# Kernel tuning notes

Measured on AMD Instinct MI355X. Metric: run time of the kernel, lower is better.

## Reference

```python
import jax, jax.numpy as jnp
import numpy as np

E = 8        # n_routed_experts
K = 2        # n_experts_per_token
H = 1024     # d_hidden
D = 512      # d_expert
NSH = 2      # n_shared_experts -> shared expert width = D*NSH


def setup_inputs() -> dict:
    key = jax.random.key(0)
    ks = jax.random.split(key, 8)
    s = 0.02
    x = jax.random.normal(ks[0], (4, 2048, H), jnp.float32)
    W_router = (jax.random.normal(ks[1], (H, E), jnp.float32) * s)
    Wg = (jax.random.normal(ks[2], (E, H, D), jnp.float32) * s)   # per-expert gate proj
    Wu = (jax.random.normal(ks[3], (E, H, D), jnp.float32) * s)   # per-expert up proj
    Wd = (jax.random.normal(ks[4], (E, D, H), jnp.float32) * s)   # per-expert down proj
    Ds = D * NSH
    Wsg = (jax.random.normal(ks[5], (H, Ds), jnp.float32) * s)
    Wsu = (jax.random.normal(ks[6], (H, Ds), jnp.float32) * s)
    Wsd = (jax.random.normal(ks[7], (Ds, H), jnp.float32) * s)
    return {"x": x, "W_router": W_router, "Wg": Wg, "Wu": Wu, "Wd": Wd,
            "Wsg": Wsg, "Wsu": Wsu, "Wsd": Wsd}


def reference(x, W_router, Wg, Wu, Wd, Wsg, Wsu, Wsd):
    B, S, Hd = x.shape
    T = B * S
    xf = x.reshape(T, Hd)

    # shared expert (SwiGLU)
    shared = (jax.nn.silu(xf @ Wsg) * (xf @ Wsu)) @ Wsd          # [T, H]

    # gating: softmax -> top-k -> renormalize
    logits = xf @ W_router                                        # [T, E]
    probs = jax.nn.softmax(logits, axis=-1)
    topk_scores, topk_idx = jax.lax.top_k(probs, K)               # [T, K]
    topk_scores = topk_scores / jnp.sum(topk_scores, axis=-1, keepdims=True)

    # combine weights: zero for unselected experts (topk indices are distinct,
    # so the original's first-match score selection equals a simple scatter)
    combine = jnp.zeros((T, E), x.dtype).at[jnp.arange(T)[:, None], topk_idx].set(topk_scores)

    # per-expert SwiGLU, computed densely and combined with sparse weights
    gate = jax.nn.silu(jnp.einsum('th,ehd->etd', xf, Wg))         # [E, T, D]
    up = jnp.einsum('th,ehd->etd', xf, Wu)                        # [E, T, D]
    expert_out = jnp.einsum('etd,edh->eth', gate * up, Wd)        # [E, T, H]
    routed = jnp.einsum('eth,te->th', expert_out, combine)        # [T, H]

    out = (routed + shared).reshape(B, S, Hd)

    # load-balancing aux loss: E * sum(mean_probs^2)
    probs_mean = jnp.mean(probs.reshape(B, S, E), axis=(0, 1))
    aux_loss = E * jnp.sum(probs_mean * probs_mean)
    return out, aux_loss
```

## Files before the change

### kernel.cpp

```cpp
#include <hip/hip_runtime.h>


typedef unsigned short u16;
typedef unsigned int   u32;
typedef short short8 __attribute__((ext_vector_type(8)));
typedef float f32x4  __attribute__((ext_vector_type(4)));

#define AS1 __attribute__((address_space(1)))
#define AS3 __attribute__((address_space(3)))

constexpr int T  = 8192;
constexpr int H  = 1024;
constexpr int E  = 8;
constexpr int D  = 512;
constexpr int DS = 1024;
constexpr int PAIR_CAP  = 17408;
constexpr int MT_ROUTED = 136;
constexpr int RB = 256;

__device__ __forceinline__ u16 f2bf(float f){
  u32 u = __builtin_bit_cast(u32, f);
  u += 0x7fffu + ((u >> 16) & 1u);
  return (u16)(u >> 16);
}
__device__ __forceinline__ float bf2f(u16 h){
  u32 u = ((u32)h) << 16;
  return __builtin_bit_cast(float, u);
}

__device__ __forceinline__ void gl_lds16(const u16* g, u16* l){
  __builtin_amdgcn_global_load_lds((const AS1 void*)g, (AS3 void*)l, 16, 0, 0);
}

__device__ __forceinline__ void wait_vmcnt8(){ __builtin_amdgcn_s_waitcnt(0x0f78); }
__device__ __forceinline__ void wait_vmcnt0(){ __builtin_amdgcn_s_waitcnt(0x0f70); }

__device__ __forceinline__ void bar_sync(){
  __builtin_amdgcn_fence(__ATOMIC_RELEASE, "workgroup", "local");
  __builtin_amdgcn_s_barrier();
  __builtin_amdgcn_fence(__ATOMIC_ACQUIRE, "workgroup", "local");
}

__device__ __forceinline__ void xcd_remap(int& mtile, int& ntile){
  int NT = gridDim.x;
  int lid = blockIdx.y * NT + blockIdx.x;
  int x8 = lid & 7, s = lid >> 3;
  mtile = x8 + 8 * (s / NT);
  ntile = s % NT;
}

template<int ISS>
struct StagePtr { const u16* p[ISS]; };

template<int ROWS>
__device__ __forceinline__ void stage_init(StagePtr<ROWS/32>& sp,
    const u16* __restrict__ gbase, int ld, int rowbase,
    const int* __restrict__ gather, int wave, int lane){
  constexpr int ISS = ROWS / 32;
  int lr = lane >> 3, ch = lane & 7;
  int chs = (ch ^ lr) * 8;
#pragma unroll
  for (int j = 0; j < ISS; ++j){
    int idx = wave * ISS + j;
    int row = idx * 8 + lr;
    int grow = gather ? gather[rowbase + row] : (rowbase + row);
    sp.p[j] = gbase + (long)grow * ld + chs;
  }
}

template<int ROWS>
__device__ __forceinline__ void stage_issue(const StagePtr<ROWS/32>& sp, int k0,
                                            u16* lds, int wave, int lane){
  constexpr int ISS = ROWS / 32;
#pragma unroll
  for (int j = 0; j < ISS; ++j)
    gl_lds16(sp.p[j] + k0, lds + (wave * ISS + j) * 512);
}

__device__ __forceinline__ int swz_off(int c, int lane){
  return ((c ^ (lane & 7)) * 8);
}

__global__ void __launch_bounds__(256) router_kernel(
    const float* __restrict__ x, const float* __restrict__ Wr,
    u16* __restrict__ xb,
    int* __restrict__ topk_idx, float* __restrict__ topk_w,
    int* __restrict__ partial_hist, float* __restrict__ partial_probs)
{
  __shared__ int   hist_s[4][8];
  __shared__ float ps_s[4][8];
  int tid = threadIdx.x, lane = tid & 63, wv = tid >> 6;
  int   histl[8] = {0,0,0,0,0,0,0,0};
  float psl[8]   = {0.f,0.f,0.f,0.f,0.f,0.f,0.f,0.f};

  for (int it = 0; it < 8; ++it){
    int t = blockIdx.x * 32 + wv * 8 + it;
    const float4* xr = (const float4*)(x + (long)t * H);
    uint2* xbr = (uint2*)(xb + (long)t * H);
    float acc[8];
#pragma unroll
    for (int e = 0; e < 8; ++e) acc[e] = 0.f;
#pragma unroll
    for (int i = 0; i < 4; ++i){
      float4 xv = xr[i * 64 + lane];
      u32 lo = (u32)f2bf(xv.x) | ((u32)f2bf(xv.y) << 16);
      u32 hi = (u32)f2bf(xv.z) | ((u32)f2bf(xv.w) << 16);
      xbr[i * 64 + lane] = make_uint2(lo, hi);
      int h0 = i * 256 + lane * 4;
#pragma unroll
      for (int j = 0; j < 4; ++j){
        float xs = (j == 0) ? xv.x : (j == 1) ? xv.y : (j == 2) ? xv.z : xv.w;
        const float4* wr = (const float4*)(Wr + (long)(h0 + j) * E);
        float4 w0 = wr[0], w1 = wr[1];
        acc[0] += xs * w0.x; acc[1] += xs * w0.y; acc[2] += xs * w0.z; acc[3] += xs * w0.w;
        acc[4] += xs * w1.x; acc[5] += xs * w1.y; acc[6] += xs * w1.z; acc[7] += xs * w1.w;
      }
    }
#pragma unroll
    for (int off = 32; off >= 1; off >>= 1){
#pragma unroll
      for (int e = 0; e < 8; ++e) acc[e] += __shfl_xor(acc[e], off, 64);
    }
    if (lane == 0){
      float m = acc[0];
#pragma unroll
      for (int e = 1; e < 8; ++e) m = fmaxf(m, acc[e]);
      float p[8], s = 0.f;
#pragma unroll
      for (int e = 0; e < 8; ++e){ p[e] = __expf(acc[e] - m); s += p[e]; }
      float inv = 1.f / s;
#pragma unroll
      for (int e = 0; e < 8; ++e) psl[e] += p[e] * inv;
      int i1 = 0; float v1 = p[0];
#pragma unroll
      for (int e = 1; e < 8; ++e) if (p[e] > v1){ v1 = p[e]; i1 = e; }
      int i2 = -1; float v2 = -1.f;
#pragma unroll
      for (int e = 0; e < 8; ++e) if (e != i1 && p[e] > v2){ v2 = p[e]; i2 = e; }
      float rs = 1.f / (v1 + v2);
      topk_idx[2 * t] = i1; topk_idx[2 * t + 1] = i2;
      topk_w[2 * t] = v1 * rs; topk_w[2 * t + 1] = v2 * rs;
      histl[i1]++; histl[i2]++;
    }
  }
  if (lane == 0){
#pragma unroll
    for (int e = 0; e < 8; ++e){ hist_s[wv][e] = histl[e]; ps_s[wv][e] = psl[e]; }
  }
  __syncthreads();
  if (tid < 8){
    int hs = 0; float ps = 0.f;
#pragma unroll
    for (int w = 0; w < 4; ++w){ hs += hist_s[w][tid]; ps += ps_s[w][tid]; }
    partial_hist[blockIdx.x * 8 + tid]  = hs;
    partial_probs[blockIdx.x * 8 + tid] = ps;
  }
}

__global__ void __launch_bounds__(64) scan_kernel(
    const int* __restrict__ partial_hist, const float* __restrict__ partial_probs,
    int* __restrict__ block_offset, float* __restrict__ out_aux)
{
  __shared__ int   csum[8][8];
  __shared__ float cps[8][8];
  __shared__ int   cbase[8][8];
  __shared__ int   base_s[8];
  int tid = threadIdx.x, e = tid & 7, c = tid >> 3;
  int s = 0; float f = 0.f;
  for (int b = c * 32; b < c * 32 + 32; ++b){
    s += partial_hist[b * 8 + e]; f += partial_probs[b * 8 + e];
  }
  csum[c][e] = s; cps[c][e] = f;
  __syncthreads();
  if (tid < 8){
    int tot = 0;
    for (int cc = 0; cc < 8; ++cc){ cbase[cc][tid] = tot; tot += csum[cc][tid]; }
    csum[0][tid] = tot;
  }
  __syncthreads();
  if (tid == 0){
    int off = 0;
    for (int ee = 0; ee < 8; ++ee){ base_s[ee] = off; off += (csum[0][ee] + 127) & ~127; }
    float a = 0.f;
    for (int ee = 0; ee < 8; ++ee){
      float ps = 0.f;
      for (int cc = 0; cc < 8; ++cc) ps += cps[cc][ee];
      float m = ps * (1.f / (float)T);
      a += m * m;
    }
    out_aux[0] = (float)E * a;
  }
  __syncthreads();
  int run = base_s[e] + cbase[c][e];
  for (int b = c * 32; b < c * 32 + 32; ++b){
    block_offset[b * 8 + e] = run;
    run += partial_hist[b * 8 + e];
  }
}

__global__ void __launch_bounds__(64) scatter_kernel(
    const int* __restrict__ topk_idx, const float* __restrict__ topk_w,
    const int* __restrict__ block_offset,
    int* __restrict__ pair_token, int* __restrict__ pair_expert,
    float* __restrict__ pair_score, int* __restrict__ token_pos)
{
  int lane = threadIdx.x, b = blockIdx.x;
  int idx = b * 64 + lane;
  int t = idx >> 1;
  int e = topk_idx[idx];
  float w = topk_w[idx];
  unsigned long long below = lane ? ((1ull << lane) - 1ull) : 0ull;
  int rank = 0, basee = 0;
#pragma unroll
  for (int ee = 0; ee < 8; ++ee){
    unsigned long long m = __ballot(e == ee);
    if (e == ee){ rank = __popcll(m & below); basee = block_offset[b * 8 + ee]; }
  }
  int pos = basee + rank;
  pair_token[pos] = t;
  pair_expert[pos] = e;
  pair_score[pos] = w;
  token_pos[idx] = pos;
}

__device__ __forceinline__ void transpose_body(const float* src, u16* dst, int R, int C,
                                               int bz){
  __shared__ float tile[32][33];
  long zoff = (long)bz * R * C;
  int tx = threadIdx.x & 31, ty = threadIdx.x >> 5;
  int c = blockIdx.x * 32 + tx;
  int rb = blockIdx.y * 32;
#pragma unroll
  for (int j = 0; j < 4; ++j)
    tile[ty + j * 8][tx] = src[zoff + (long)(rb + ty + j * 8) * C + c];
  __syncthreads();
#pragma unroll
  for (int j = 0; j < 4; ++j){
    int cc = blockIdx.x * 32 + ty + j * 8;
    dst[zoff + (long)cc * R + rb + tx] = f2bf(tile[tx][ty + j * 8]);
  }
}

__global__ void __launch_bounds__(256) transpose_kernel(const float* __restrict__ src,
                                                        u16* __restrict__ dst, int R, int C){
  transpose_body(src, dst, R, C, blockIdx.z);
}

__global__ void __launch_bounds__(256) transpose2_kernel(
    const float* __restrict__ s0, u16* __restrict__ d0,
    const float* __restrict__ s1, u16* __restrict__ d1, int R, int C, int Z){
  int z = blockIdx.z;
  if (z < Z) transpose_body(s0, d0, R, C, z);
  else       transpose_body(s1, d1, R, C, z - Z);
}

__global__ void __launch_bounds__(256) transpose3_kernel(
    const float* __restrict__ s0, u16* __restrict__ d0,
    const float* __restrict__ s1, u16* __restrict__ d1,
    const float* __restrict__ s2, u16* __restrict__ d2, int R, int C){
  int z = blockIdx.z;
  const float* s = (z == 0) ? s0 : (z == 1) ? s1 : s2;
  u16* d = (z == 0) ? d0 : (z == 1) ? d1 : d2;
  transpose_body(s, d, R, C, 0);
}

__global__ void __launch_bounds__(256) gateup_kernel(
    const u16* __restrict__ A, const u16* __restrict__ Bg, const u16* __restrict__ Bu,
    u16* __restrict__ Hout, int N, int K,
    const int* __restrict__ gather, const int* __restrict__ pexp, long bstride)
{
  __shared__ u16 As[2][128 * 64];
  __shared__ u16 Bgs[2][64 * 64];
  __shared__ u16 Bus[2][64 * 64];
  int tid = threadIdx.x, lane = tid & 63, wave = tid >> 6;
  int wy = wave >> 1, wx = wave & 1;
  int mtile, ntile; xcd_remap(mtile, ntile);
  int m0 = mtile * 128, n0 = ntile * 64;
  int e = pexp ? pexp[m0] : 0;
  const u16* bg = Bg + (long)e * bstride;
  const u16* bu = Bu + (long)e * bstride;
  int rl = lane & 15, q = lane >> 4;

  StagePtr<4> spA; StagePtr<2> spG; StagePtr<2> spU;
  stage_init<128>(spA, A, K, m0, gather, wave, lane);
  stage_init<64>(spG, bg, K, n0, nullptr, wave, lane);
  stage_init<64>(spU, bu, K, n0, nullptr, wave, lane);

  f32x4 accG[4][2], accU[4][2];
#pragma unroll
  for (int i = 0; i < 4; ++i)
#pragma unroll
    for (int j = 0; j < 2; ++j)
#pragma unroll
      for (int r = 0; r < 4; ++r){ accG[i][j][r] = 0.f; accU[i][j][r] = 0.f; }

  stage_issue<128>(spA, 0, As[0], wave, lane);
  stage_issue<64>(spG, 0, Bgs[0], wave, lane);
  stage_issue<64>(spU, 0, Bus[0], wave, lane);

  int NI = K / 64;
  for (int i = 0; i < NI; ++i){
    int cur = i & 1, nxt = cur ^ 1;
    if (i + 1 < NI){
      int kn = (i + 1) * 64;
      stage_issue<128>(spA, kn, As[nxt], wave, lane);
      stage_issue<64>(spG, kn, Bgs[nxt], wave, lane);
      stage_issue<64>(spU, kn, Bus[nxt], wave, lane);
      wait_vmcnt8();
    } else {
      wait_vmcnt0();
    }
    bar_sync();
#pragma unroll
    for (int ks = 0; ks < 2; ++ks){
      int off = swz_off(ks * 4 + q, lane);
      short8 a[4], g2[2], u2[2];
#pragma unroll
      for (int mt = 0; mt < 4; ++mt)
        a[mt] = *(const short8*)(As[cur] + (wy * 64 + mt * 16 + rl) * 64 + off);
#pragma unroll
      for (int nt = 0; nt < 2; ++nt){
        g2[nt] = *(const short8*)(Bgs[cur] + (wx * 32 + nt * 16 + rl) * 64 + off);
        u2[nt] = *(const short8*)(Bus[cur] + (wx * 32 + nt * 16 + rl) * 64 + off);
      }
#pragma unroll
      for (int mt = 0; mt < 4; ++mt)
#pragma unroll
        for (int nt = 0; nt < 2; ++nt){
          accG[mt][nt] = __builtin_amdgcn_mfma_f32_16x16x32_bf16(a[mt], g2[nt], accG[mt][nt], 0, 0, 0);
          accU[mt][nt] = __builtin_amdgcn_mfma_f32_16x16x32_bf16(a[mt], u2[nt], accU[mt][nt], 0, 0, 0);
        }
    }
    if (i + 1 < NI) bar_sync();
  }
  int row0 = m0 + wy * 64, col0 = n0 + wx * 32;
#pragma unroll
  for (int mt = 0; mt < 4; ++mt)
#pragma unroll
    for (int nt = 0; nt < 2; ++nt)
#pragma unroll
      for (int r = 0; r < 4; ++r){
        int row = row0 + mt * 16 + q * 4 + r;
        int col = col0 + nt * 16 + rl;
        float g = accG[mt][nt][r], u = accU[mt][nt][r];
        float h = g / (1.f + __expf(-g)) * u;
        Hout[(long)row * N + col] = f2bf(h);
      }
}

template<bool ROUTED>
__device__ __forceinline__ void down_body(
    const u16* __restrict__ A, const u16* __restrict__ Bbase, int K,
    u16* __restrict__ rout, const float* __restrict__ pair_score,
    const int* __restrict__ token_pos, float* __restrict__ out)
{
  __shared__ u16 As[2][128 * 64];
  __shared__ u16 Bs[2][128 * 64];
  int tid = threadIdx.x, lane = tid & 63, wave = tid >> 6;
  int wy = wave >> 1, wx = wave & 1;
  int mtile, ntile; xcd_remap(mtile, ntile);
  int m0 = mtile * 128, n0 = ntile * 128;
  int rl = lane & 15, q = lane >> 4;

  StagePtr<4> spA, spB;
  stage_init<128>(spA, A, K, m0, nullptr, wave, lane);
  stage_init<128>(spB, Bbase, K, n0, nullptr, wave, lane);

  f32x4 acc[4][4];
#pragma unroll
  for (int i = 0; i < 4; ++i)
#pragma unroll
    for (int j = 0; j < 4; ++j)
#pragma unroll
      for (int r = 0; r < 4; ++r) acc[i][j][r] = 0.f;

  stage_issue<128>(spA, 0, As[0], wave, lane);
  stage_issue<128>(spB, 0, Bs[0], wave, lane);

  int NI = K / 64;
  for (int i = 0; i < NI; ++i){
    int cur = i & 1, nxt = cur ^ 1;
    if (i + 1 < NI){
      int kn = (i + 1) * 64;
      stage_issue<128>(spA, kn, As[nxt], wave, lane);
      stage_issue<128>(spB, kn, Bs[nxt], wave, lane);
      wait_vmcnt8();
    } else {
      wait_vmcnt0();
    }
    bar_sync();
#pragma unroll
    for (int ks = 0; ks < 2; ++ks){
      int off = swz_off(ks * 4 + q, lane);
      short8 a[4], bv[4];
#pragma unroll
      for (int mt = 0; mt < 4; ++mt)
        a[mt] = *(const short8*)(As[cur] + (wy * 64 + mt * 16 + rl) * 64 + off);
#pragma unroll
      for (int nt = 0; nt < 4; ++nt)
        bv[nt] = *(const short8*)(Bs[cur] + (wx * 64 + nt * 16 + rl) * 64 + off);
#pragma unroll
      for (int mt = 0; mt < 4; ++mt)
#pragma unroll
        for (int nt = 0; nt < 4; ++nt)
          acc[mt][nt] = __builtin_amdgcn_mfma_f32_16x16x32_bf16(a[mt], bv[nt], acc[mt][nt], 0, 0, 0);
    }
    if (i + 1 < NI) bar_sync();
  }
#pragma unroll
  for (int mt = 0; mt < 4; ++mt)
#pragma unroll
    for (int r = 0; r < 4; ++r){
      int row = m0 + wy * 64 + mt * 16 + q * 4 + r;
      if (ROUTED){
        float s = pair_score[row];
        long rbase = (long)row * H;
#pragma unroll
        for (int nt = 0; nt < 4; ++nt){
          int col = n0 + wx * 64 + nt * 16 + rl;
          rout[rbase + col] = f2bf(s * acc[mt][nt][r]);
        }
      } else {
        int p0 = token_pos[2 * row], p1 = token_pos[2 * row + 1];
        long o = (long)row * H;
#pragma unroll
        for (int nt = 0; nt < 4; ++nt){
          int col = n0 + wx * 64 + nt * 16 + rl;
          out[o + col] = acc[mt][nt][r]
                       + bf2f(rout[(long)p0 * H + col])
                       + bf2f(rout[(long)p1 * H + col]);
        }
      }
    }
}

__global__ void __launch_bounds__(256) down_routed_kernel(
    const u16* __restrict__ A, const u16* __restrict__ B, u16* __restrict__ rout,
    const float* __restrict__ pair_score, const int* __restrict__ pexp)
{
  int NT = gridDim.x;
  int lid = blockIdx.y * NT + blockIdx.x;
  int x8 = lid & 7, s = lid >> 3;
  int mtile = x8 + 8 * (s / NT);
  int e = pexp[mtile * 128];
  down_body<true>(A, B + (long)e * (H * D), D, rout, pair_score, nullptr, nullptr);
}

__global__ void __launch_bounds__(256) down_shared_kernel(
    const u16* __restrict__ A, const u16* __restrict__ B,
    const u16* __restrict__ rout, const int* __restrict__ token_pos,
    float* __restrict__ out)
{
  down_body<false>(A, B, DS, const_cast<u16*>(rout), nullptr, token_pos, out);
}

extern "C" void kernel_launch(void* const* d_in, const int* in_sizes, int n_in,
                              void* d_out, int out_size, void* d_ws, size_t ws_size,
                              hipStream_t stream)
{
  (void)in_sizes; (void)n_in; (void)out_size; (void)ws_size;
  const float* x   = (const float*)d_in[0];
  const float* Wr  = (const float*)d_in[1];
  const float* Wg  = (const float*)d_in[2];
  const float* Wu  = (const float*)d_in[3];
  const float* Wd  = (const float*)d_in[4];
  const float* Wsg = (const float*)d_in[5];
  const float* Wsu = (const float*)d_in[6];
  const float* Wsd = (const float*)d_in[7];
  float* out = (float*)d_out;

  char* ws = (char*)d_ws;
  size_t off = 0;
  auto alloc = [&](size_t bytes) -> void* {
    void* p = ws + off; off += (bytes + 255) & ~(size_t)255; return p;
  };
  u16* xb   = (u16*)alloc((size_t)T * H * 2);
  u16* WsgT = (u16*)alloc((size_t)DS * H * 2);
  u16* WsuT = (u16*)alloc((size_t)DS * H * 2);
  u16* WsdT = (u16*)alloc((size_t)H * DS * 2);
  u16* WgT  = (u16*)alloc((size_t)E * D * H * 2);
  u16* WuT  = (u16*)alloc((size_t)E * D * H * 2);
  u16* WdT  = (u16*)alloc((size_t)E * H * D * 2);
  u16* hs   = (u16*)alloc((size_t)T * DS * 2);
  u16* hr   = (u16*)alloc((size_t)PAIR_CAP * D * 2);
  u16* rout = (u16*)alloc((size_t)PAIR_CAP * H * 2);
  int*   topk_idx  = (int*)alloc((size_t)T * 2 * 4);
  float* topk_w    = (float*)alloc((size_t)T * 2 * 4);
  int*   token_pos = (int*)alloc((size_t)T * 2 * 4);
  int*   partial_hist  = (int*)alloc((size_t)RB * 8 * 4);
  float* partial_probs = (float*)alloc((size_t)RB * 8 * 4);
  int*   block_offset  = (int*)alloc((size_t)RB * 8 * 4);
  char* zbase = ws + off;
  int*   pair_token  = (int*)alloc((size_t)PAIR_CAP * 4);
  int*   pair_expert = (int*)alloc((size_t)PAIR_CAP * 4);
  float* pair_score  = (float*)alloc((size_t)PAIR_CAP * 4);
  size_t zbytes = (size_t)((ws + off) - zbase);

  hipMemsetAsync(zbase, 0, zbytes, stream);

  transpose3_kernel<<<dim3(32, 32, 3), 256, 0, stream>>>(
      Wsg, WsgT, Wsu, WsuT, Wsd, WsdT, 1024, 1024);
  transpose2_kernel<<<dim3(D / 32, H / 32, 2 * E), 256, 0, stream>>>(
      Wg, WgT, Wu, WuT, H, D, E);
  transpose_kernel<<<dim3(H / 32, D / 32, E), 256, 0, stream>>>(Wd, WdT, D, H);

  router_kernel<<<RB, 256, 0, stream>>>(x, Wr, xb, topk_idx, topk_w,
                                        partial_hist, partial_probs);
  scan_kernel<<<1, 64, 0, stream>>>(partial_hist, partial_probs, block_offset,
                                    out + (size_t)T * H);
  scatter_kernel<<<RB, 64, 0, stream>>>(topk_idx, topk_w, block_offset,
                                        pair_token, pair_expert, pair_score, token_pos);

  gateup_kernel<<<dim3(DS / 64, T / 128), 256, 0, stream>>>(
      xb, WsgT, WsuT, hs, DS, H, nullptr, nullptr, 0);
  gateup_kernel<<<dim3(D / 64, MT_ROUTED), 256, 0, stream>>>(
      xb, WgT, WuT, hr, D, H, pair_token, pair_expert, (long)D * H);
  down_routed_kernel<<<dim3(H / 128, MT_ROUTED), 256, 0, stream>>>(
      hr, WdT, rout, pair_score, pair_expert);
  down_shared_kernel<<<dim3(H / 128, T / 128), 256, 0, stream>>>(
      hs, WsdT, rout, token_pos, out);
}
```

Measured before the change: 329.9 us.

## Fuse shared/routed GEMMs into single launches and combine outputs via atomics

Merges the shared and routed gate/up GEMMs into one launch, and the shared and routed down GEMMs into another, using a flat block id to pick the branch. The bf16 routed-output buffer and token_pos gather are removed: both down paths now accumulate directly into a zeroed fp32 output with atomic adds. Router and scatter blocks are halved in size (RB 512) for more parallelism in the small kernels. The intent is fewer launches, better load balance across the GPU and less intermediate traffic, at the cost of an extra output memset, atomic contention, and summation order that is no longer deterministic.

Result: slower. 463.4 us (+40.4%).

```diff
diff --git a/kernel.cpp b/kernel.cpp
--- a/kernel.cpp
+++ b/kernel.cpp
@@ -16,17 +16,18 @@
 constexpr int DS = 1024;
 constexpr int PAIR_CAP  = 17408;
 constexpr int MT_ROUTED = 136;
-constexpr int RB = 256;
+constexpr int RB = 512;
+
+constexpr int GU_ROUTED_BLKS = 8 * MT_ROUTED;
+constexpr int GU_SHARED_BLKS = 16 * (T / 128);
+constexpr int DN_SHARED_BLKS = 8 * (T / 128);
+constexpr int DN_ROUTED_BLKS = 8 * MT_ROUTED;
 
 __device__ __forceinline__ u16 f2bf(float f){
   u32 u = __builtin_bit_cast(u32, f);
   u += 0x7fffu + ((u >> 16) & 1u);
   return (u16)(u >> 16);
 }
-__device__ __forceinline__ float bf2f(u16 h){
-  u32 u = ((u32)h) << 16;
-  return __builtin_bit_cast(float, u);
-}
 
 __device__ __forceinline__ void gl_lds16(const u16* g, u16* l){
   __builtin_amdgcn_global_load_lds((const AS1 void*)g, (AS3 void*)l, 16, 0, 0);
@@ -39,14 +40,6 @@
   __builtin_amdgcn_fence(__ATOMIC_RELEASE, "workgroup", "local");
   __builtin_amdgcn_s_barrier();
   __builtin_amdgcn_fence(__ATOMIC_ACQUIRE, "workgroup", "local");
-}
-
-__device__ __forceinline__ void xcd_remap(int& mtile, int& ntile){
-  int NT = gridDim.x;
-  int lid = blockIdx.y * NT + blockIdx.x;
-  int x8 = lid & 7, s = lid >> 3;
-  mtile = x8 + 8 * (s / NT);
-  ntile = s % NT;
 }
 
 template<int ISS>
@@ -93,8 +86,8 @@
   int   histl[8] = {0,0,0,0,0,0,0,0};
   float psl[8]   = {0.f,0.f,0.f,0.f,0.f,0.f,0.f,0.f};
 
-  for (int it = 0; it < 8; ++it){
-    int t = blockIdx.x * 32 + wv * 8 + it;
+  for (int it = 0; it < 4; ++it){
+    int t = blockIdx.x * 16 + wv * 4 + it;
     const float4* xr = (const float4*)(x + (long)t * H);
     uint2* xbr = (uint2*)(xb + (long)t * H);
     float acc[8];
@@ -167,7 +160,7 @@
   __shared__ int   base_s[8];
   int tid = threadIdx.x, e = tid & 7, c = tid >> 3;
   int s = 0; float f = 0.f;
-  for (int b = c * 32; b < c * 32 + 32; ++b){
+  for (int b = c * 64; b < c * 64 + 64; ++b){
     s += partial_hist[b * 8 + e]; f += partial_probs[b * 8 + e];
   }
   csum[c][e] = s; cps[c][e] = f;
@@ -192,7 +185,7 @@
   }
   __syncthreads();
   int run = base_s[e] + cbase[c][e];
-  for (int b = c * 32; b < c * 32 + 32; ++b){
+  for (int b = c * 64; b < c * 64 + 64; ++b){
     block_offset[b * 8 + e] = run;
     run += partial_hist[b * 8 + e];
   }
@@ -202,10 +195,11 @@
     const int* __restrict__ topk_idx, const float* __restrict__ topk_w,
     const int* __restrict__ block_offset,
     int* __restrict__ pair_token, int* __restrict__ pair_expert,
-    float* __restrict__ pair_score, int* __restrict__ token_pos)
+    float* __restrict__ pair_score)
 {
   int lane = threadIdx.x, b = blockIdx.x;
-  int idx = b * 64 + lane;
+  if (lane >= 32) return;
+  int idx = b * 32 + lane;
   int t = idx >> 1;
   int e = topk_idx[idx];
   float w = topk_w[idx];
@@ -220,7 +214,6 @@
   pair_token[pos] = t;
   pair_expert[pos] = e;
   pair_score[pos] = w;
-  token_pos[idx] = pos;
 }
 
 __device__ __forceinline__ void transpose_body(const float* src, u16* dst, int R, int C,
@@ -264,27 +257,21 @@
   transpose_body(s, d, R, C, 0);
 }
 
-__global__ void __launch_bounds__(256) gateup_kernel(
+__device__ __forceinline__ void gateup_body(
     const u16* __restrict__ A, const u16* __restrict__ Bg, const u16* __restrict__ Bu,
     u16* __restrict__ Hout, int N, int K,
-    const int* __restrict__ gather, const int* __restrict__ pexp, long bstride)
-{
-  __shared__ u16 As[2][128 * 64];
-  __shared__ u16 Bgs[2][64 * 64];
-  __shared__ u16 Bus[2][64 * 64];
+    const int* __restrict__ gather, int mtile, int ntile,
+    u16 (*As)[128 * 64], u16 (*Bgs)[64 * 64], u16 (*Bus)[64 * 64])
+{
   int tid = threadIdx.x, lane = tid & 63, wave = tid >> 6;
   int wy = wave >> 1, wx = wave & 1;
-  int mtile, ntile; xcd_remap(mtile, ntile);
   int m0 = mtile * 128, n0 = ntile * 64;
-  int e = pexp ? pexp[m0] : 0;
-  const u16* bg = Bg + (long)e * bstride;
-  const u16* bu = Bu + (long)e * bstride;
   int rl = lane & 15, q = lane >> 4;
 
   StagePtr<4> spA; StagePtr<2> spG; StagePtr<2> spU;
   stage_init<128>(spA, A, K, m0, gather, wave, lane);
-  stage_init<64>(spG, bg, K, n0, nullptr, wave, lane);
-  stage_init<64>(spU, bu, K, n0, nullptr, wave, lane);
+  stage_init<64>(spG, Bg, K, n0, nullptr, wave, lane);
+  stage_init<64>(spU, Bu, K, n0, nullptr, wave, lane);
 
   f32x4 accG[4][2], accU[4][2];
 #pragma unroll
@@ -348,23 +335,45 @@
       }
 }
 
+__global__ void __launch_bounds__(256) gateup_fused(
+    const u16* __restrict__ xb,
+    const u16* __restrict__ WgT, const u16* __restrict__ WuT, u16* __restrict__ hr,
+    const u16* __restrict__ WsgT, const u16* __restrict__ WsuT, u16* __restrict__ hs,
+    const int* __restrict__ pair_token, const int* __restrict__ pair_expert)
+{
+  __shared__ u16 As[2][128 * 64];
+  __shared__ u16 Bgs[2][64 * 64];
+  __shared__ u16 Bus[2][64 * 64];
+  int fid = blockIdx.x;
+  if (fid < GU_ROUTED_BLKS){
+    int x8 = fid & 7, s = fid >> 3;
+    int mtile = x8 + 8 * (s >> 3), ntile = s & 7;
+    int e = pair_expert[mtile * 128];
+    gateup_body(xb, WgT + (long)e * (D * H), WuT + (long)e * (D * H), hr,
+                D, H, pair_token, mtile, ntile, As, Bgs, Bus);
+  } else {
+    int lid = fid - GU_ROUTED_BLKS;
+    int x8 = lid & 7, s = lid >> 3;
+    int mtile = x8 + 8 * (s >> 4), ntile = s & 15;
+    gateup_body(xb, WsgT, WsuT, hs, DS, H, nullptr, mtile, ntile, As, Bgs, Bus);
+  }
+}
+
 template<bool ROUTED>
 __device__ __forceinline__ void down_body(
-    const u16* __restrict__ A, const u16* __restrict__ Bbase, int K,
-    u16* __restrict__ rout, const float* __restrict__ pair_score,
-    const int* __restrict__ token_pos, float* __restrict__ out)
-{
-  __shared__ u16 As[2][128 * 64];
-  __shared__ u16 Bs[2][128 * 64];
+    const u16* __restrict__ A, const u16* __restrict__ B, int K,
+    const float* __restrict__ pair_score, const int* __restrict__ pair_token,
+    float* __restrict__ out, int mtile, int ntile,
+    u16 (*As)[128 * 64], u16 (*Bs)[128 * 64])
+{
   int tid = threadIdx.x, lane = tid & 63, wave = tid >> 6;
   int wy = wave >> 1, wx = wave & 1;
-  int mtile, ntile; xcd_remap(mtile, ntile);
   int m0 = mtile * 128, n0 = ntile * 128;
   int rl = lane & 15, q = lane >> 4;
 
   StagePtr<4> spA, spB;
   stage_init<128>(spA, A, K, m0, nullptr, wave, lane);
-  stage_init<128>(spB, Bbase, K, n0, nullptr, wave, lane);
+  stage_init<128>(spB, B, K, n0, nullptr, wave, lane);
 
   f32x4 acc[4][4];
 #pragma unroll
@@ -414,44 +423,45 @@
       int row = m0 + wy * 64 + mt * 16 + q * 4 + r;
       if (ROUTED){
         float s = pair_score[row];
-        long rbase = (long)row * H;
+        int tok = pair_token[row];
+        float* o = out + (long)tok * H;
 #pragma unroll
         for (int nt = 0; nt < 4; ++nt){
           int col = n0 + wx * 64 + nt * 16 + rl;
-          rout[rbase + col] = f2bf(s * acc[mt][nt][r]);
+          unsafeAtomicAdd(o + col, s * acc[mt][nt][r]);
         }
       } else {
-        int p0 = token_pos[2 * row], p1 = token_pos[2 * row + 1];
-        long o = (long)row * H;
+        float* o = out + (long)row * H;
 #pragma unroll
         for (int nt = 0; nt < 4; ++nt){
           int col = n0 + wx * 64 + nt * 16 + rl;
-          out[o + col] = acc[mt][nt][r]
-                       + bf2f(rout[(long)p0 * H + col])
-                       + bf2f(rout[(long)p1 * H + col]);
+          unsafeAtomicAdd(o + col, acc[mt][nt][r]);
         }
       }
     }
 }
 
-__global__ void __launch_bounds__(256) down_routed_kernel(
-    const u16* __restrict__ A, const u16* __restrict__ B, u16* __restrict__ rout,
-    const float* __restrict__ pair_score, const int* __restrict__ pexp)
-{
-  int NT = gridDim.x;
-  int lid = blockIdx.y * NT + blockIdx.x;
-  int x8 = lid & 7, s = lid >> 3;
-  int mtile = x8 + 8 * (s / NT);
-  int e = pexp[mtile * 128];
-  down_body<true>(A, B + (long)e * (H * D), D, rout, pair_score, nullptr, nullptr);
-}
-
-__global__ void __launch_bounds__(256) down_shared_kernel(
-    const u16* __restrict__ A, const u16* __restrict__ B,
-    const u16* __restrict__ rout, const int* __restrict__ token_pos,
-    float* __restrict__ out)
-{
-  down_body<false>(A, B, DS, const_cast<u16*>(rout), nullptr, token_pos, out);
+__global__ void __launch_bounds__(256) down_fused(
+    const u16* __restrict__ hs, const u16* __restrict__ WsdT,
+    const u16* __restrict__ hr, const u16* __restrict__ WdT,
+    const float* __restrict__ pair_score, const int* __restrict__ pair_token,
+    const int* __restrict__ pair_expert, float* __restrict__ out)
+{
+  __shared__ u16 As[2][128 * 64];
+  __shared__ u16 Bs[2][128 * 64];
+  int fid = blockIdx.x;
+  if (fid < DN_SHARED_BLKS){
+    int x8 = fid & 7, s = fid >> 3;
+    int mtile = x8 + 8 * (s >> 3), ntile = s & 7;
+    down_body<false>(hs, WsdT, DS, nullptr, nullptr, out, mtile, ntile, As, Bs);
+  } else {
+    int lid = fid - DN_SHARED_BLKS;
+    int x8 = lid & 7, s = lid >> 3;
+    int mtile = x8 + 8 * (s >> 3), ntile = s & 7;
+    int e = pair_expert[mtile * 128];
+    down_body<true>(hr, WdT + (long)e * (H * D), D, pair_score, pair_token,
+                    out, mtile, ntile, As, Bs);
+  }
 }
 
 extern "C" void kernel_launch(void* const* d_in, const int* in_sizes, int n_in,
@@ -483,10 +493,8 @@
   u16* WdT  = (u16*)alloc((size_t)E * H * D * 2);
   u16* hs   = (u16*)alloc((size_t)T * DS * 2);
   u16* hr   = (u16*)alloc((size_t)PAIR_CAP * D * 2);
-  u16* rout = (u16*)alloc((size_t)PAIR_CAP * H * 2);
   int*   topk_idx  = (int*)alloc((size_t)T * 2 * 4);
   float* topk_w    = (float*)alloc((size_t)T * 2 * 4);
-  int*   token_pos = (int*)alloc((size_t)T * 2 * 4);
   int*   partial_hist  = (int*)alloc((size_t)RB * 8 * 4);
   float* partial_probs = (float*)alloc((size_t)RB * 8 * 4);
   int*   block_offset  = (int*)alloc((size_t)RB * 8 * 4);
@@ -497,6 +505,7 @@
   size_t zbytes = (size_t)((ws + off) - zbase);
 
   hipMemsetAsync(zbase, 0, zbytes, stream);
+  hipMemsetAsync(out, 0, (size_t)T * H * 4, stream);
 
   transpose3_kernel<<<dim3(32, 32, 3), 256, 0, stream>>>(
       Wsg, WsgT, Wsu, WsuT, Wsd, WsdT, 1024, 1024);
@@ -509,14 +518,11 @@
   scan_kernel<<<1, 64, 0, stream>>>(partial_hist, partial_probs, block_offset,
                                     out + (size_t)T * H);
   scatter_kernel<<<RB, 64, 0, stream>>>(topk_idx, topk_w, block_offset,
-                                        pair_token, pair_expert, pair_score, token_pos);
-
-  gateup_kernel<<<dim3(DS / 64, T / 128), 256, 0, stream>>>(
-      xb, WsgT, WsuT, hs, DS, H, nullptr, nullptr, 0);
-  gateup_kernel<<<dim3(D / 64, MT_ROUTED), 256, 0, stream>>>(
-      xb, WgT, WuT, hr, D, H, pair_token, pair_expert, (long)D * H);
-  down_routed_kernel<<<dim3(H / 128, MT_ROUTED), 256, 0, stream>>>(
-      hr, WdT, rout, pair_score, pair_expert);
-  down_shared_kernel<<<dim3(H / 128, T / 128), 256, 0, stream>>>(
-      hs, WsdT, rout, token_pos, out);
-}
+                                        pair_token, pair_expert, pair_score);
+
+  gateup_fused<<<GU_ROUTED_BLKS + GU_SHARED_BLKS, 256, 0, stream>>>(
+      xb, WgT, WuT, hr, WsgT, WsuT, hs, pair_token, pair_expert);
+
+  down_fused<<<DN_SHARED_BLKS + DN_ROUTED_BLKS, 256, 0, stream>>>(
+      hs, WsdT, hr, WdT, pair_score, pair_token, pair_expert, out);
+}
```
